# Optimization experiments

Measured on AMD Instinct MI355X. Metric: run time of the kernel, lower is better.

The kernel has to match this reference:

```python
import jax, jax.numpy as jnp
import numpy as np

N_NODES = 50000
N_EDGES = 800000
X_DIM = 32
E_DIM = 32
HID = 64
OUT = 32


def setup_inputs() -> dict:
    key = jax.random.key(0)
    ks = jax.random.split(key, 6)
    x = jax.random.normal(ks[0], (N_NODES, X_DIM), dtype=jnp.float32)
    edge_index = jax.random.randint(ks[1], (2, N_EDGES), 0, N_NODES, dtype=jnp.int64)
    edge_attr = jax.random.normal(ks[2], (N_EDGES, E_DIM), dtype=jnp.float32)
    in_dim = 2 * X_DIM + E_DIM  # 96
    W1 = jax.random.normal(ks[3], (in_dim, HID), dtype=jnp.float32) * (1.0 / np.sqrt(in_dim))
    b1 = jnp.zeros((HID,), dtype=jnp.float32)
    W2 = jax.random.normal(ks[4], (HID, OUT), dtype=jnp.float32) * (1.0 / np.sqrt(HID))
    b2 = jnp.zeros((OUT,), dtype=jnp.float32)
    return {"x": x, "edge_index": edge_index, "edge_attr": edge_attr,
            "W1": W1, "b1": b1, "W2": W2, "b2": b2}


def reference(x, edge_index, edge_attr, W1, b1, W2, b2):
    num_nodes = x.shape[0]
    rol, col = edge_index[0], edge_index[1]
    # gather endpoint features + edge attr -> [E, 2*x_dim + e_dim]
    e_feat = jnp.concatenate([x[rol], x[col], edge_attr], axis=-1)
    # 2-layer MLP (ReLU hidden)
    h = jax.nn.relu(e_feat @ W1 + b1)
    v = h @ W2 + b2  # [E, OUT]
    # scatter-max aggregation into destination nodes (empty segments -> -inf)
    x_cand = jax.ops.segment_max(v, col, num_segments=num_nodes)
    # elementwise max residual against trailing slice of x
    return jnp.maximum(x_cand, x[:, -v.shape[-1]:])
```

## Files before the change

kernel.cpp:

```cpp
#include <hip/hip_runtime.h>


constexpr int XD   = 32;
constexpr int HID  = 64;
constexpr int OUTD = 32;
constexpr int BM   = 128;
constexpr int HSTR = 72;
constexpr int BIN_SHIFT = 5;
constexpr int BINW  = 1 << BIN_SHIFT;
constexpr int BLK_E = 8192;
constexpr int EPB   = BLK_E / 256;

typedef __attribute__((ext_vector_type(8)))  short    short8;
typedef __attribute__((ext_vector_type(4)))  float    f32x4;
typedef __attribute__((ext_vector_type(4)))  float    floatx4;
typedef __attribute__((ext_vector_type(2)))  unsigned u32x2;

static __device__ __forceinline__ unsigned f2bf(float f) {
    union { float f; unsigned u; } x; x.f = f;
    unsigned r = x.u + 0x7fff + ((x.u >> 16) & 1);
    return r >> 16;
}
static __device__ __forceinline__ unsigned encf(float f) {
    unsigned u = __float_as_uint(f);
    return (u >> 31) ? ~u : (u | 0x80000000u);
}
static __device__ __forceinline__ float decf(unsigned k) {
    return __uint_as_float((k >> 31) ? (k & 0x7fffffffu) : ~k);
}

__global__ __launch_bounds__(256) void prep_hist(
    const float* __restrict__ x, unsigned* __restrict__ xbf,
    const float* __restrict__ W1, const float* __restrict__ W2,
    unsigned* __restrict__ w1s, unsigned* __restrict__ w2s,
    const int* __restrict__ ei, unsigned* __restrict__ cnt,
    int n_edges, int nbins, int nblk, int total8)
{
    __shared__ unsigned lh[2048];
    const int t = threadIdx.x;
    const int b = blockIdx.x;

    if (b < nblk) {
        for (int i = t; i < nbins; i += 256) lh[i] = 0u;
        __syncthreads();
        const int chunk = b * BLK_E;
#pragma unroll
        for (int i = 0; i < EPB; ++i) {
            const int e = chunk + i * 256 + t;
            if (e < n_edges)
                atomicAdd(&lh[((unsigned)ei[n_edges + e]) >> BIN_SHIFT], 1u);
        }
        __syncthreads();
        for (int i = t; i < nbins; i += 256)
            cnt[(size_t)b * nbins + i] = lh[i];
        return;
    }

    const int i = (b - nblk) * 256 + t;

    if (i < total8) {
        const float4* src = reinterpret_cast<const float4*>(x) + (size_t)i * 2;
        float4 a = src[0], bb = src[1];
        uint4 o;
        o.x = f2bf(a.x)  | (f2bf(a.y)  << 16);
        o.y = f2bf(a.z)  | (f2bf(a.w)  << 16);
        o.z = f2bf(bb.x) | (f2bf(bb.y) << 16);
        o.w = f2bf(bb.z) | (f2bf(bb.w) << 16);
        reinterpret_cast<uint4*>(xbf)[i] = o;
    }

    if (i < 768) {
        const int ti = i >> 6, lane = i & 63;
        const int nt = ti / 3, ks = ti % 3;
        const int col = nt * 16 + (lane & 15);
        const int k0  = ks * 32 + ((lane >> 4) << 3);
        unsigned o[4];
#pragma unroll
        for (int p = 0; p < 4; ++p)
            o[p] = f2bf(W1[(k0 + 2 * p) * HID + col]) |
                   (f2bf(W1[(k0 + 2 * p + 1) * HID + col]) << 16);
        reinterpret_cast<uint4*>(w1s)[i] = make_uint4(o[0], o[1], o[2], o[3]);
    } else if (i < 1024) {
        const int tt = i - 768;
        const int ti = tt >> 6, lane = tt & 63;
        const int nt = ti >> 1, ks = ti & 1;
        const int col = nt * 16 + (lane & 15);
        const int k0  = ks * 32 + ((lane >> 4) << 3);
        unsigned o[4];
#pragma unroll
        for (int p = 0; p < 4; ++p)
            o[p] = f2bf(W2[(k0 + 2 * p) * OUTD + col]) |
                   (f2bf(W2[(k0 + 2 * p + 1) * OUTD + col]) << 16);
        reinterpret_cast<uint4*>(w2s)[tt] = make_uint4(o[0], o[1], o[2], o[3]);
    }
}

__global__ __launch_bounds__(128) void bin_off(
    const unsigned* __restrict__ cnt, unsigned* __restrict__ off,
    unsigned* __restrict__ totals, int nblk, int nbins)
{
    __shared__ unsigned ts[128];
    const int j = blockIdx.x;
    const int t = threadIdx.x;
    const unsigned d = (t < nblk) ? cnt[(size_t)t * nbins + j] : 0u;
    ts[t] = d;
    __syncthreads();
#pragma unroll
    for (int o = 1; o < 128; o <<= 1) {
        unsigned v = (t >= o) ? ts[t - o] : 0u;
        __syncthreads();
        ts[t] += v;
        __syncthreads();
    }
    if (t < nblk) off[(size_t)t * nbins + j] = ts[t] - d;
    if (t == 127) totals[j] = ts[127];
}

__global__ __launch_bounds__(256) void base_scan(
    const unsigned* __restrict__ totals, unsigned* __restrict__ base, int nbins)
{
    __shared__ unsigned ts[256];
    const int t = threadIdx.x;
    unsigned d[8];
    unsigned s = 0;
#pragma unroll
    for (int k = 0; k < 8; ++k) {
        const int i = t * 8 + k;
        d[k] = (i < nbins) ? totals[i] : 0u;
        s += d[k];
    }
    ts[t] = s;
    __syncthreads();
#pragma unroll
    for (int o = 1; o < 256; o <<= 1) {
        unsigned v = (t >= o) ? ts[t - o] : 0u;
        __syncthreads();
        ts[t] += v;
        __syncthreads();
    }
    unsigned run = (t == 0) ? 0u : ts[t - 1];
#pragma unroll
    for (int k = 0; k < 8; ++k) {
        const int i = t * 8 + k;
        if (i < nbins) base[i] = run;
        run += d[k];
    }
    if (t == 255) base[nbins] = run;
}

__global__ __launch_bounds__(256) void bin_write(
    const int* __restrict__ ei, const unsigned* __restrict__ off,
    const unsigned* __restrict__ base, unsigned* __restrict__ rec,
    int n_edges, int nbins)
{
    __shared__ unsigned loff[2048];
    __shared__ unsigned lrank[2048];
    const int t = threadIdx.x;
    const int b = blockIdx.x;
    for (int i = t; i < nbins; i += 256) {
        loff[i]  = base[i] + off[(size_t)b * nbins + i];
        lrank[i] = 0u;
    }
    __syncthreads();
    const int chunk = b * BLK_E;
#pragma unroll
    for (int i = 0; i < EPB; ++i) {
        const int e = chunk + i * 256 + t;
        if (e < n_edges) {
            const unsigned row = (unsigned)ei[e];
            const unsigned col = (unsigned)ei[n_edges + e];
            const unsigned bin = col >> BIN_SHIFT;
            const unsigned r   = atomicAdd(&lrank[bin], 1u);
            const unsigned pos = loff[bin] + r;
            u32x2 v; v.x = (row << 16) | col; v.y = (unsigned)e;
            *reinterpret_cast<u32x2*>(rec + (size_t)pos * 2) = v;
        }
    }
}

__global__ __launch_bounds__(256) void edge_mlp_fused(
    const unsigned* __restrict__ xbf,
    const unsigned* __restrict__ rec,
    const float*    __restrict__ ea,
    const unsigned* __restrict__ w1s,
    const unsigned* __restrict__ w2s,
    const float*    __restrict__ b1,
    const float*    __restrict__ b2,
    const float*    __restrict__ x,
    const unsigned* __restrict__ base,
    float*          __restrict__ out,
    int n_edges, int n_nodes)
{
    __shared__ alignas(16) unsigned short Hlds[BM * HSTR];
    __shared__ unsigned accK[BINW * OUTD];

    const int t    = threadIdx.x;
    const int lane = t & 63;
    const int wave = t >> 6;
    const int bin  = blockIdx.x;
    const int n0   = bin << BIN_SHIFT;

    const unsigned sbeg = base[bin];
    const unsigned send = base[bin + 1];

    short8 w1f[12];
#pragma unroll
    for (int ti = 0; ti < 12; ++ti)
        w1f[ti] = *reinterpret_cast<const short8*>(w1s + (size_t)(ti * 64 + lane) * 4);
    short8 w2f[4];
#pragma unroll
    for (int ti = 0; ti < 4; ++ti)
        w2f[ti] = *reinterpret_cast<const short8*>(w2s + (size_t)(ti * 64 + lane) * 4);
    float bb1[4];
#pragma unroll
    for (int nt = 0; nt < 4; ++nt) bb1[nt] = b1[nt * 16 + (lane & 15)];
    float bb2[2];
#pragma unroll
    for (int nt = 0; nt < 2; ++nt) bb2[nt] = b2[nt * 16 + (lane & 15)];

#pragma unroll
    for (int k = 0; k < (BINW * OUTD) / 256; ++k) {
        const int idx = t + k * 256;
        const int g   = n0 + (idx >> 5);
        const float r = (g < n_nodes) ? x[(size_t)g * XD + (idx & 31)] : 0.0f;
        accK[idx] = encf(r);
    }
    __syncthreads();

    const int ntile = (int)(send - sbeg + BM - 1) / BM;
    const int koff  = lane >> 4;

    for (int tile = 0; tile < ntile; ++tile) {
        u32x2 q; q.x = 0u; q.y = 0u;
        if (lane < 32) {
            unsigned p = sbeg + (unsigned)tile * BM + (unsigned)wave * 32 + (unsigned)lane;
            if (p >= send) p = send - 1;
            q = __builtin_nontemporal_load(
                reinterpret_cast<const u32x2*>(rec + (size_t)p * 2));
        }

        f32x4 acc1[2][4];
#pragma unroll
        for (int mi = 0; mi < 2; ++mi)
#pragma unroll
            for (int nt = 0; nt < 4; ++nt) acc1[mi][nt] = (f32x4){0.f, 0.f, 0.f, 0.f};

#pragma unroll
        for (int mi = 0; mi < 2; ++mi) {
            const int s = mi * 16 + (lane & 15);
            const unsigned rcp = (unsigned)__shfl((int)q.x, s, 64);
            const unsigned eid = (unsigned)__shfl((int)q.y, s, 64);
            const unsigned idR = rcp >> 16;
            const unsigned idC = rcp & 0xffffu;

            const short8 aR = *reinterpret_cast<const short8*>(
                xbf + (size_t)idR * 16 + koff * 4);
            const short8 aC = *reinterpret_cast<const short8*>(
                xbf + (size_t)idC * 16 + koff * 4);
            const floatx4* ep = reinterpret_cast<const floatx4*>(
                ea + (size_t)eid * 32 + koff * 8);
            const floatx4 e0 = __builtin_nontemporal_load(ep);
            const floatx4 e1 = __builtin_nontemporal_load(ep + 1);
            union { uint4 u; short8 s8; } ae;
            ae.u.x = f2bf(e0.x) | (f2bf(e0.y) << 16);
            ae.u.y = f2bf(e0.z) | (f2bf(e0.w) << 16);
            ae.u.z = f2bf(e1.x) | (f2bf(e1.y) << 16);
            ae.u.w = f2bf(e1.z) | (f2bf(e1.w) << 16);

#pragma unroll
            for (int nt = 0; nt < 4; ++nt) {
                acc1[mi][nt] = __builtin_amdgcn_mfma_f32_16x16x32_bf16(
                    aR, w1f[nt * 3 + 0], acc1[mi][nt], 0, 0, 0);
                acc1[mi][nt] = __builtin_amdgcn_mfma_f32_16x16x32_bf16(
                    aC, w1f[nt * 3 + 1], acc1[mi][nt], 0, 0, 0);
                acc1[mi][nt] = __builtin_amdgcn_mfma_f32_16x16x32_bf16(
                    ae.s8, w1f[nt * 3 + 2], acc1[mi][nt], 0, 0, 0);
            }
        }

#pragma unroll
        for (int mi = 0; mi < 2; ++mi) {
            const int mt = wave * 2 + mi;
#pragma unroll
            for (int nt = 0; nt < 4; ++nt)
#pragma unroll
                for (int r = 0; r < 4; ++r) {
                    const float h = fmaxf(acc1[mi][nt][r] + bb1[nt], 0.0f);
                    Hlds[(mt * 16 + ((lane >> 4) << 2) + r) * HSTR + nt * 16 + (lane & 15)] =
                        (unsigned short)f2bf(h);
                }
        }

        f32x4 acc2[2][2];
#pragma unroll
        for (int mi = 0; mi < 2; ++mi)
#pragma unroll
            for (int nt = 0; nt < 2; ++nt) acc2[mi][nt] = (f32x4){0.f, 0.f, 0.f, 0.f};
#pragma unroll
        for (int ks = 0; ks < 2; ++ks) {
#pragma unroll
            for (int mi = 0; mi < 2; ++mi) {
                const int mt = wave * 2 + mi;
                short8 hfrag = *reinterpret_cast<const short8*>(
                    &Hlds[(mt * 16 + (lane & 15)) * HSTR + ks * 32 + ((lane >> 4) << 3)]);
#pragma unroll
                for (int nt = 0; nt < 2; ++nt)
                    acc2[mi][nt] = __builtin_amdgcn_mfma_f32_16x16x32_bf16(
                        hfrag, w2f[nt * 2 + ks], acc2[mi][nt], 0, 0, 0);
            }
        }

#pragma unroll
        for (int mi = 0; mi < 2; ++mi) {
#pragma unroll
            for (int r = 0; r < 4; ++r) {
                const int rowl = mi * 16 + ((lane >> 4) << 2) + r;
                const unsigned rcp = (unsigned)__shfl((int)q.x, rowl, 64);
                const int ln = (int)(rcp & 0xffffu) - n0;
#pragma unroll
                for (int nt = 0; nt < 2; ++nt) {
                    const float val = acc2[mi][nt][r] + bb2[nt];
                    atomicMax(&accK[ln * OUTD + nt * 16 + (lane & 15)], encf(val));
                }
            }
        }
    }

    __syncthreads();
#pragma unroll
    for (int k = 0; k < (BINW * OUTD) / 256; ++k) {
        const int idx = t + k * 256;
        const int g   = n0 + (idx >> 5);
        if (g < n_nodes)
            out[(size_t)g * OUTD + (idx & 31)] = decf(accK[idx]);
    }
}

extern "C" void kernel_launch(void* const* d_in, const int* in_sizes, int n_in,
                              void* d_out, int out_size, void* d_ws, size_t ws_size,
                              hipStream_t stream)
{
    const float* x  = (const float*)d_in[0];
    const int*   ei = (const int*)  d_in[1];
    const float* ea = (const float*)d_in[2];
    const float* W1 = (const float*)d_in[3];
    const float* b1 = (const float*)d_in[4];
    const float* W2 = (const float*)d_in[5];
    const float* b2 = (const float*)d_in[6];
    float* out = (float*)d_out;

    const int n_nodes = in_sizes[0] / XD;
    const int n_edges = in_sizes[2] / 32;
    const int nbins   = (n_nodes + BINW - 1) >> BIN_SHIFT;
    const int nblk    = (n_edges + BLK_E - 1) / BLK_E;

    size_t off_b = 0;
    unsigned* cnt    = (unsigned*)((char*)d_ws + off_b); off_b += (size_t)nblk * nbins * 4;
    unsigned* offm   = (unsigned*)((char*)d_ws + off_b); off_b += (size_t)nblk * nbins * 4;
    unsigned* totals = (unsigned*)((char*)d_ws + off_b); off_b += (size_t)nbins * 4;
    unsigned* basep  = (unsigned*)((char*)d_ws + off_b); off_b += (size_t)(nbins + 1) * 4;
    off_b = (off_b + 15) & ~(size_t)15;
    unsigned* rec    = (unsigned*)((char*)d_ws + off_b); off_b += (size_t)n_edges * 8;
    unsigned* xbf    = (unsigned*)((char*)d_ws + off_b); off_b += (size_t)n_nodes * 16 * 4;
    unsigned* w1s    = (unsigned*)((char*)d_ws + off_b); off_b += 768 * 16;
    unsigned* w2s    = (unsigned*)((char*)d_ws + off_b);

    const int total8     = n_nodes * XD / 8;
    const int prep_blk   = (max(total8, 1024) + 255) / 256;

    prep_hist<<<nblk + prep_blk, 256, 0, stream>>>(
        x, xbf, W1, W2, w1s, w2s, ei, cnt, n_edges, nbins, nblk, total8);
    bin_off<<<nbins, 128, 0, stream>>>(cnt, offm, totals, nblk, nbins);
    base_scan<<<1, 256, 0, stream>>>(totals, basep, nbins);
    bin_write<<<nblk, 256, 0, stream>>>(ei, offm, basep, rec, n_edges, nbins);
    edge_mlp_fused<<<nbins, 256, 0, stream>>>(
        xbf, rec, ea, w1s, w2s, b1, b2, x, basep, out, n_edges, n_nodes);
}
```

Measured before the change: 99.84 us.

## Software-pipeline edge-record and edge-attribute loads across tiles

Restructures the per-tile loop so edge records are prefetched two tiles ahead and edge attributes one tile ahead, held in registers and rotated at the end of each iteration. The aim is to hide the latency of the irregular global loads behind the MFMA and atomic work of the current tile. The extra live registers for the prefetched attribute fragments and records may lower occupancy.

```diff
diff --git a/kernel.cpp b/kernel.cpp
--- a/kernel.cpp
+++ b/kernel.cpp
@@ -230,7 +230,7 @@
     const int ntile = (int)(send - sbeg + BM - 1) / BM;
     const int koff  = lane >> 4;
 
-    for (int tile = 0; tile < ntile; ++tile) {
+    auto rec_load = [&](int tile) -> u32x2 {
         u32x2 q; q.x = 0u; q.y = 0u;
         if (lane < 32) {
             unsigned p = sbeg + (unsigned)tile * BM + (unsigned)wave * 32 + (unsigned)lane;
@@ -238,18 +238,43 @@
             q = __builtin_nontemporal_load(
                 reinterpret_cast<const u32x2*>(rec + (size_t)p * 2));
         }
-
-        f32x4 acc1[2][4];
-#pragma unroll
-        for (int mi = 0; mi < 2; ++mi)
-#pragma unroll
-            for (int nt = 0; nt < 4; ++nt) acc1[mi][nt] = (f32x4){0.f, 0.f, 0.f, 0.f};
-
+        return q;
+    };
+    auto ea_issue = [&](const u32x2& q, floatx4 eg[2][2]) {
 #pragma unroll
         for (int mi = 0; mi < 2; ++mi) {
             const int s = mi * 16 + (lane & 15);
-            const unsigned rcp = (unsigned)__shfl((int)q.x, s, 64);
             const unsigned eid = (unsigned)__shfl((int)q.y, s, 64);
+            const floatx4* ep = reinterpret_cast<const floatx4*>(
+                ea + (size_t)eid * 32 + koff * 8);
+            eg[mi][0] = __builtin_nontemporal_load(ep);
+            eg[mi][1] = __builtin_nontemporal_load(ep + 1);
+        }
+    };
+
+    u32x2 qc, qn;
+    floatx4 egc[2][2], egn[2][2];
+    if (ntile > 0) {
+        qc = rec_load(0);
+        ea_issue(qc, egc);
+        qn = (ntile > 1) ? rec_load(1) : qc;
+    }
+
+    for (int tile = 0; tile < ntile; ++tile) {
+        if (tile + 1 < ntile) ea_issue(qn, egn);
+        u32x2 q2 = qn;
+        if (tile + 2 < ntile) q2 = rec_load(tile + 2);
+
+        f32x4 acc1[2][4];
+#pragma unroll
+        for (int mi = 0; mi < 2; ++mi)
+#pragma unroll
+            for (int nt = 0; nt < 4; ++nt) acc1[mi][nt] = (f32x4){0.f, 0.f, 0.f, 0.f};
+
+#pragma unroll
+        for (int mi = 0; mi < 2; ++mi) {
+            const int s = mi * 16 + (lane & 15);
+            const unsigned rcp = (unsigned)__shfl((int)qc.x, s, 64);
             const unsigned idR = rcp >> 16;
             const unsigned idC = rcp & 0xffffu;
 
@@ -257,10 +282,8 @@
                 xbf + (size_t)idR * 16 + koff * 4);
             const short8 aC = *reinterpret_cast<const short8*>(
                 xbf + (size_t)idC * 16 + koff * 4);
-            const floatx4* ep = reinterpret_cast<const floatx4*>(
-                ea + (size_t)eid * 32 + koff * 8);
-            const floatx4 e0 = __builtin_nontemporal_load(ep);
-            const floatx4 e1 = __builtin_nontemporal_load(ep + 1);
+            const floatx4 e0 = egc[mi][0];
+            const floatx4 e1 = egc[mi][1];
             union { uint4 u; short8 s8; } ae;
             ae.u.x = f2bf(e0.x) | (f2bf(e0.y) << 16);
             ae.u.y = f2bf(e0.z) | (f2bf(e0.w) << 16);
@@ -315,7 +338,7 @@
 #pragma unroll
             for (int r = 0; r < 4; ++r) {
                 const int rowl = mi * 16 + ((lane >> 4) << 2) + r;
-                const unsigned rcp = (unsigned)__shfl((int)q.x, rowl, 64);
+                const unsigned rcp = (unsigned)__shfl((int)qc.x, rowl, 64);
                 const int ln = (int)(rcp & 0xffffu) - n0;
 #pragma unroll
                 for (int nt = 0; nt < 2; ++nt) {
@@ -323,6 +346,13 @@
                     atomicMax(&accK[ln * OUTD + nt * 16 + (lane & 15)], encf(val));
                 }
             }
+        }
+
+        qc = qn; qn = q2;
+#pragma unroll
+        for (int mi = 0; mi < 2; ++mi) {
+            egc[mi][0] = egn[mi][0];
+            egc[mi][1] = egn[mi][1];
         }
     }
 
```

Result: slower. 110.1 us (+10.3%).

## Pre-permute edge attributes into bf16 in bin order during bin_write

Applied to the files above, without the earlier changes.

bin_write now reads each edge's fp32 attributes coalesced by edge id, converts them to bf16 and writes them at the binned position, so the MLP kernel reads contiguous bf16 rows instead of gathering scattered fp32 rows. The per-edge record shrinks from two words to one because the edge id is no longer needed. In exchange, bin_write does an extra 128 B read and a 64 B scattered write per edge, and its loop is no longer unrolled.

```diff
diff --git a/kernel.cpp b/kernel.cpp
--- a/kernel.cpp
+++ b/kernel.cpp
@@ -14,7 +14,6 @@
 typedef __attribute__((ext_vector_type(8)))  short    short8;
 typedef __attribute__((ext_vector_type(4)))  float    f32x4;
 typedef __attribute__((ext_vector_type(4)))  float    floatx4;
-typedef __attribute__((ext_vector_type(2)))  unsigned u32x2;
 
 static __device__ __forceinline__ unsigned f2bf(float f) {
     union { float f; unsigned u; } x; x.f = f;
@@ -149,8 +148,10 @@
 }
 
 __global__ __launch_bounds__(256) void bin_write(
-    const int* __restrict__ ei, const unsigned* __restrict__ off,
-    const unsigned* __restrict__ base, unsigned* __restrict__ rec,
+    const int* __restrict__ ei, const float* __restrict__ ea,
+    const unsigned* __restrict__ off, const unsigned* __restrict__ base,
+    unsigned* __restrict__ rec4,
+    unsigned short* __restrict__ eabf,
     int n_edges, int nbins)
 {
     __shared__ unsigned loff[2048];
@@ -163,7 +164,7 @@
     }
     __syncthreads();
     const int chunk = b * BLK_E;
-#pragma unroll
+#pragma unroll 1
     for (int i = 0; i < EPB; ++i) {
         const int e = chunk + i * 256 + t;
         if (e < n_edges) {
@@ -172,16 +173,29 @@
             const unsigned bin = col >> BIN_SHIFT;
             const unsigned r   = atomicAdd(&lrank[bin], 1u);
             const unsigned pos = loff[bin] + r;
-            u32x2 v; v.x = (row << 16) | col; v.y = (unsigned)e;
-            *reinterpret_cast<u32x2*>(rec + (size_t)pos * 2) = v;
+            rec4[pos] = (row << 16) | col;
+
+            const floatx4* ep = reinterpret_cast<const floatx4*>(ea + (size_t)e * 32);
+            uint4* dst = reinterpret_cast<uint4*>(eabf + (size_t)pos * 32);
+#pragma unroll
+            for (int qq = 0; qq < 4; ++qq) {
+                const floatx4 f0 = ep[2 * qq];
+                const floatx4 f1 = ep[2 * qq + 1];
+                uint4 o;
+                o.x = f2bf(f0.x) | (f2bf(f0.y) << 16);
+                o.y = f2bf(f0.z) | (f2bf(f0.w) << 16);
+                o.z = f2bf(f1.x) | (f2bf(f1.y) << 16);
+                o.w = f2bf(f1.z) | (f2bf(f1.w) << 16);
+                dst[qq] = o;
+            }
         }
     }
 }
 
 __global__ __launch_bounds__(256) void edge_mlp_fused(
-    const unsigned* __restrict__ xbf,
-    const unsigned* __restrict__ rec,
-    const float*    __restrict__ ea,
+    const unsigned*       __restrict__ xbf,
+    const unsigned*       __restrict__ rec4,
+    const unsigned short* __restrict__ eabf,
     const unsigned* __restrict__ w1s,
     const unsigned* __restrict__ w2s,
     const float*    __restrict__ b1,
@@ -231,12 +245,11 @@
     const int koff  = lane >> 4;
 
     for (int tile = 0; tile < ntile; ++tile) {
-        u32x2 q; q.x = 0u; q.y = 0u;
-        if (lane < 32) {
-            unsigned p = sbeg + (unsigned)tile * BM + (unsigned)wave * 32 + (unsigned)lane;
+        unsigned qx = 0u;
+        {
+            unsigned p = sbeg + (unsigned)tile * BM + (unsigned)wave * 32 + (unsigned)(lane & 31);
             if (p >= send) p = send - 1;
-            q = __builtin_nontemporal_load(
-                reinterpret_cast<const u32x2*>(rec + (size_t)p * 2));
+            if (lane < 32) qx = __builtin_nontemporal_load(rec4 + p);
         }
 
         f32x4 acc1[2][4];
@@ -248,8 +261,7 @@
 #pragma unroll
         for (int mi = 0; mi < 2; ++mi) {
             const int s = mi * 16 + (lane & 15);
-            const unsigned rcp = (unsigned)__shfl((int)q.x, s, 64);
-            const unsigned eid = (unsigned)__shfl((int)q.y, s, 64);
+            const unsigned rcp = (unsigned)__shfl((int)qx, s, 64);
             const unsigned idR = rcp >> 16;
             const unsigned idC = rcp & 0xffffu;
 
@@ -257,15 +269,11 @@
                 xbf + (size_t)idR * 16 + koff * 4);
             const short8 aC = *reinterpret_cast<const short8*>(
                 xbf + (size_t)idC * 16 + koff * 4);
-            const floatx4* ep = reinterpret_cast<const floatx4*>(
-                ea + (size_t)eid * 32 + koff * 8);
-            const floatx4 e0 = __builtin_nontemporal_load(ep);
-            const floatx4 e1 = __builtin_nontemporal_load(ep + 1);
-            union { uint4 u; short8 s8; } ae;
-            ae.u.x = f2bf(e0.x) | (f2bf(e0.y) << 16);
-            ae.u.y = f2bf(e0.z) | (f2bf(e0.w) << 16);
-            ae.u.z = f2bf(e1.x) | (f2bf(e1.y) << 16);
-            ae.u.w = f2bf(e1.z) | (f2bf(e1.w) << 16);
+            unsigned epos = sbeg + (unsigned)tile * BM + (unsigned)wave * 32
+                          + (unsigned)(mi * 16) + (unsigned)(lane & 15);
+            if (epos >= send) epos = send - 1;
+            const short8 aE = *reinterpret_cast<const short8*>(
+                eabf + (size_t)epos * 32 + koff * 8);
 
 #pragma unroll
             for (int nt = 0; nt < 4; ++nt) {
@@ -274,7 +282,7 @@
                 acc1[mi][nt] = __builtin_amdgcn_mfma_f32_16x16x32_bf16(
                     aC, w1f[nt * 3 + 1], acc1[mi][nt], 0, 0, 0);
                 acc1[mi][nt] = __builtin_amdgcn_mfma_f32_16x16x32_bf16(
-                    ae.s8, w1f[nt * 3 + 2], acc1[mi][nt], 0, 0, 0);
+                    aE, w1f[nt * 3 + 2], acc1[mi][nt], 0, 0, 0);
             }
         }
 
@@ -315,7 +323,7 @@
 #pragma unroll
             for (int r = 0; r < 4; ++r) {
                 const int rowl = mi * 16 + ((lane >> 4) << 2) + r;
-                const unsigned rcp = (unsigned)__shfl((int)q.x, rowl, 64);
+                const unsigned rcp = (unsigned)__shfl((int)qx, rowl, 64);
                 const int ln = (int)(rcp & 0xffffu) - n0;
 #pragma unroll
                 for (int nt = 0; nt < 2; ++nt) {
@@ -359,8 +367,10 @@
     unsigned* offm   = (unsigned*)((char*)d_ws + off_b); off_b += (size_t)nblk * nbins * 4;
     unsigned* totals = (unsigned*)((char*)d_ws + off_b); off_b += (size_t)nbins * 4;
     unsigned* basep  = (unsigned*)((char*)d_ws + off_b); off_b += (size_t)(nbins + 1) * 4;
-    off_b = (off_b + 15) & ~(size_t)15;
-    unsigned* rec    = (unsigned*)((char*)d_ws + off_b); off_b += (size_t)n_edges * 8;
+    off_b = (off_b + 63) & ~(size_t)63;
+    unsigned* rec4   = (unsigned*)((char*)d_ws + off_b); off_b += (size_t)n_edges * 4;
+    off_b = (off_b + 63) & ~(size_t)63;
+    unsigned short* eabf = (unsigned short*)((char*)d_ws + off_b); off_b += (size_t)n_edges * 64;
     unsigned* xbf    = (unsigned*)((char*)d_ws + off_b); off_b += (size_t)n_nodes * 16 * 4;
     unsigned* w1s    = (unsigned*)((char*)d_ws + off_b); off_b += 768 * 16;
     unsigned* w2s    = (unsigned*)((char*)d_ws + off_b);
@@ -372,7 +382,7 @@
         x, xbf, W1, W2, w1s, w2s, ei, cnt, n_edges, nbins, nblk, total8);
     bin_off<<<nbins, 128, 0, stream>>>(cnt, offm, totals, nblk, nbins);
     base_scan<<<1, 256, 0, stream>>>(totals, basep, nbins);
-    bin_write<<<nblk, 256, 0, stream>>>(ei, offm, basep, rec, n_edges, nbins);
+    bin_write<<<nblk, 256, 0, stream>>>(ei, ea, offm, basep, rec4, eabf, n_edges, nbins);
     edge_mlp_fused<<<nbins, 256, 0, stream>>>(
-        xbf, rec, ea, w1s, w2s, b1, b2, x, basep, out, n_edges, n_nodes);
-}
+        xbf, rec4, eabf, w1s, w2s, b1, b2, x, basep, out, n_edges, n_nodes);
+}
```

Measured after the change: 150.6 us. 50.9% more time.
